# Kernel tuning notes

Hardware: AMD Instinct MI355X
Metric: run time of the kernel (lower is better)

The kernel has to match this reference:

```python
import jax, jax.numpy as jnp
import numpy as np

N = 200000  # nodes
C = 256     # per-node feature dim

def setup_inputs() -> dict:
    key = jax.random.key(0)
    k1, k2, k3, k4, k5, k6, k7 = jax.random.split(key, 7)
    out1 = jax.random.normal(k1, (N, C), dtype=jnp.float32)
    out2 = jax.random.normal(k2, (N, C), dtype=jnp.float32)
    neighbour = jax.random.randint(k3, (N, 3), 0, N, dtype=jnp.int64)
    # Combination2: Conv1d(512,512,1) == Linear(512->512)
    W_comb = jax.random.normal(k4, (512, 2 * C), dtype=jnp.float32) * (1.0 / np.sqrt(2 * C))
    b_comb = jax.random.normal(k5, (512,), dtype=jnp.float32) * 0.01
    # Aggregation2: Conv1d(256,512,1) == Linear(256->512)
    W_agg = jax.random.normal(k6, (512, C), dtype=jnp.float32) * (1.0 / np.sqrt(C))
    b_agg = jax.random.normal(k7, (512,), dtype=jnp.float32) * 0.01
    return {"out1": out1, "out2": out2, "neighbour": neighbour,
            "W_comb": W_comb, "b_comb": b_comb, "W_agg": W_agg, "b_agg": b_agg}


def reference(out1, out2, neighbour, W_comb, b_comb, W_agg, b_agg):
    # Combination2: concat features then 1x1 conv (per-node linear)
    a1 = jnp.concatenate([out1, out2], axis=1)              # [N, 512]
    out3 = jnp.einsum('nc,oc->no', a1, W_comb) + b_comb     # [N, 512]

    # Aggregation2: mean of self + 3 gathered neighbors, then linear 256->512
    neigh_feats = jnp.take(out2, neighbour, axis=0)          # [N, 3, C]
    agg = (out2 + neigh_feats.sum(axis=1)) * 0.25            # [N, C]
    out4 = jnp.einsum('nc,oc->no', agg, W_agg) + b_agg       # [N, 512]
    return (out3, out4)
```

## Files before the change

### kernel.cpp

```cpp
#include <hip/hip_runtime.h>


typedef __bf16 bf16x8 __attribute__((ext_vector_type(8)));
typedef float f32x4 __attribute__((ext_vector_type(4)));

#define N_NODES 200000
#define BM 64
#define NTILES (N_NODES / BM)
#define ROWC 520
#define ROWA 264
#define GRID_B 2048

__device__ __forceinline__ unsigned short f2bf(float x) {
  union { float f; unsigned int u; } v; v.f = x;
  return (unsigned short)((v.u + 0x7FFFu + ((v.u >> 16) & 1u)) >> 16);
}

__device__ __forceinline__ void st_bf4(unsigned short* p, float4 f) {
  uint2 w;
  w.x = (unsigned int)f2bf(f.x) | ((unsigned int)f2bf(f.y) << 16);
  w.y = (unsigned int)f2bf(f.z) | ((unsigned int)f2bf(f.w) << 16);
  *reinterpret_cast<uint2*>(p) = w;
}

__global__ void pack_w_kernel(const float* __restrict__ Wc,
                              const float* __restrict__ Wa,
                              unsigned short* __restrict__ Pc,
                              unsigned short* __restrict__ Pa) {
  int t = blockIdx.x * 256 + threadIdx.x;
  if (t >= (512 + 256) * 64) return;
  int lane = t & 63;
  int tile = t >> 6;
  const float* W;
  unsigned short* P;
  int K, kt_n;
  if (tile < 512) { W = Wc; P = Pc; K = 512; kt_n = 16; }
  else { tile -= 512; W = Wa; P = Pa; K = 256; kt_n = 8; }
  int nt = tile / kt_n;
  int kt = tile - nt * kt_n;
  int row = nt * 16 + (lane & 15);
  int k0 = kt * 32 + (lane >> 4) * 8;
  const float* src = W + (size_t)row * K + k0;
  unsigned short* dst = P + (size_t)tile * 512 + lane * 8;
#pragma unroll
  for (int j = 0; j < 8; ++j) dst[j] = f2bf(src[j]);
}

__global__ __launch_bounds__(512, 4) void gemm_kernel(
    const float* __restrict__ out1, const float* __restrict__ out2,
    const unsigned short* __restrict__ Pc, const unsigned short* __restrict__ Pa,
    const float* __restrict__ b_comb,
    float* __restrict__ out3, unsigned short* __restrict__ Y) {
  __shared__ unsigned short Acomb[BM * ROWC];

  const int tid = threadIdx.x;
  const int ln8 = tid >> 3, c8 = tid & 7;
  const int wave = tid >> 6, lane = tid & 63;
  const int l15 = lane & 15, l4 = lane >> 4;
  const long long node0 = (long long)blockIdx.x * BM;

  float bcv[4];
#pragma unroll
  for (int n = 0; n < 4; ++n) bcv[n] = b_comb[wave * 64 + n * 16 + l15];

  {
    const size_t gn = (size_t)node0 + ln8;
    const float4* r1 = reinterpret_cast<const float4*>(out1 + gn * 256);
    const float4* r2 = reinterpret_cast<const float4*>(out2 + gn * 256);
#pragma unroll
    for (int r = 0; r < 8; ++r) {
      const int cc = c8 + 8 * r;
      st_bf4(&Acomb[ln8 * ROWC + cc * 4], r1[cc]);
      st_bf4(&Acomb[ln8 * ROWC + 256 + cc * 4], r2[cc]);
    }
  }
  __syncthreads();

  const int nt0 = wave * 4;

  {
    f32x4 acc[4][4];
#pragma unroll
    for (int m = 0; m < 4; ++m)
#pragma unroll
      for (int n = 0; n < 4; ++n) acc[m][n] = (f32x4){0.f, 0.f, 0.f, 0.f};

    const unsigned short* pc = Pc + (size_t)nt0 * 16 * 512 + lane * 8;
    const unsigned short* ab = &Acomb[(size_t)l15 * ROWC + l4 * 8];
#pragma unroll
    for (int kt = 0; kt < 16; ++kt) {
      bf16x8 bfr[4];
#pragma unroll
      for (int n = 0; n < 4; ++n)
        bfr[n] = *reinterpret_cast<const bf16x8*>(pc + ((size_t)n * 16 + kt) * 512);
      bf16x8 av[4];
#pragma unroll
      for (int m = 0; m < 4; ++m)
        av[m] = *reinterpret_cast<const bf16x8*>(ab + (size_t)m * 16 * ROWC + kt * 32);
#pragma unroll
      for (int m = 0; m < 4; ++m)
#pragma unroll
        for (int n = 0; n < 4; ++n)
          acc[m][n] = __builtin_amdgcn_mfma_f32_16x16x32_bf16(av[m], bfr[n], acc[m][n], 0, 0, 0);
    }
    float* o3 = out3 + node0 * 512 + wave * 64 + l15;
#pragma unroll
    for (int m = 0; m < 4; ++m)
#pragma unroll
      for (int r = 0; r < 4; ++r) {
        float* p = o3 + (long long)(m * 16 + l4 * 4 + r) * 512;
#pragma unroll
        for (int n = 0; n < 4; ++n) p[n * 16] = acc[m][n][r] + bcv[n];
      }
  }

  {
    f32x4 acc[4][4];
#pragma unroll
    for (int m = 0; m < 4; ++m)
#pragma unroll
      for (int n = 0; n < 4; ++n) acc[m][n] = (f32x4){0.f, 0.f, 0.f, 0.f};

    const unsigned short* pa = Pa + (size_t)nt0 * 8 * 512 + lane * 8;
    const unsigned short* ab = &Acomb[(size_t)l15 * ROWC + 256 + l4 * 8];
#pragma unroll
    for (int kt = 0; kt < 8; ++kt) {
      bf16x8 bfr[4];
#pragma unroll
      for (int n = 0; n < 4; ++n)
        bfr[n] = *reinterpret_cast<const bf16x8*>(pa + ((size_t)n * 8 + kt) * 512);
      bf16x8 av[4];
#pragma unroll
      for (int m = 0; m < 4; ++m)
        av[m] = *reinterpret_cast<const bf16x8*>(ab + (size_t)m * 16 * ROWC + kt * 32);
#pragma unroll
      for (int m = 0; m < 4; ++m)
#pragma unroll
        for (int n = 0; n < 4; ++n)
          acc[m][n] = __builtin_amdgcn_mfma_f32_16x16x32_bf16(av[m], bfr[n], acc[m][n], 0, 0, 0);
    }

    __syncthreads();
#pragma unroll
    for (int m = 0; m < 4; ++m)
#pragma unroll
      for (int r = 0; r < 4; ++r) {
        const int row = m * 16 + l4 * 4 + r;
#pragma unroll
        for (int n = 0; n < 4; ++n)
          Acomb[row * ROWC + wave * 64 + n * 16 + l15] = f2bf(acc[m][n][r]);
      }
    __syncthreads();

    {
      const unsigned short* src = &Acomb[ln8 * ROWC];
      unsigned short* dst = Y + (node0 + ln8) * 512;
#pragma unroll
      for (int j = 0; j < 8; ++j) {
        const int e = (c8 + 8 * j) * 8;
        *reinterpret_cast<uint4*>(dst + e) = *reinterpret_cast<const uint4*>(src + e);
      }
    }
  }
}

__device__ __forceinline__ float bf_lo(unsigned u) {
  union { unsigned x; float f; } c; c.x = u << 16; return c.f;
}
__device__ __forceinline__ float bf_hi(unsigned u) {
  union { unsigned x; float f; } c; c.x = u & 0xFFFF0000u; return c.f;
}

__global__ __launch_bounds__(256) void gather_kernel(
    const unsigned short* __restrict__ Y, const int* __restrict__ nbr,
    const float* __restrict__ b_agg, float* __restrict__ out4) {
  const int lane = threadIdx.x & 63;
  const int wid = (blockIdx.x * 256 + threadIdx.x) >> 6;
  const int nwaves = (GRID_B * 256) >> 6;

  float ba[8];
  const float* bp = b_agg + lane * 8;
#pragma unroll
  for (int j = 0; j < 8; ++j) ba[j] = bp[j];

  for (int n = wid; n < N_NODES; n += nwaves) {
    int i0 = nbr[3 * n + 0];
    int i1 = nbr[3 * n + 1];
    int i2 = nbr[3 * n + 2];
    i0 = i0 < 0 ? 0 : (i0 >= N_NODES ? N_NODES - 1 : i0);
    i1 = i1 < 0 ? 0 : (i1 >= N_NODES ? N_NODES - 1 : i1);
    i2 = i2 < 0 ? 0 : (i2 >= N_NODES ? N_NODES - 1 : i2);

    const uint4 a  = *reinterpret_cast<const uint4*>(Y + (size_t)n  * 512 + lane * 8);
    const uint4 b0 = *reinterpret_cast<const uint4*>(Y + (size_t)i0 * 512 + lane * 8);
    const uint4 b1 = *reinterpret_cast<const uint4*>(Y + (size_t)i1 * 512 + lane * 8);
    const uint4 b2 = *reinterpret_cast<const uint4*>(Y + (size_t)i2 * 512 + lane * 8);

    const unsigned wa[4] = {a.x, a.y, a.z, a.w};
    const unsigned w0[4] = {b0.x, b0.y, b0.z, b0.w};
    const unsigned w1[4] = {b1.x, b1.y, b1.z, b1.w};
    const unsigned w2[4] = {b2.x, b2.y, b2.z, b2.w};
    float s[8];
#pragma unroll
    for (int w = 0; w < 4; ++w) {
      s[2 * w]     = bf_lo(wa[w]) + bf_lo(w0[w]) + bf_lo(w1[w]) + bf_lo(w2[w]);
      s[2 * w + 1] = bf_hi(wa[w]) + bf_hi(w0[w]) + bf_hi(w1[w]) + bf_hi(w2[w]);
    }
    f32x4 o0 = {s[0] * 0.25f + ba[0], s[1] * 0.25f + ba[1],
                s[2] * 0.25f + ba[2], s[3] * 0.25f + ba[3]};
    f32x4 o1 = {s[4] * 0.25f + ba[4], s[5] * 0.25f + ba[5],
                s[6] * 0.25f + ba[6], s[7] * 0.25f + ba[7]};
    f32x4* op = reinterpret_cast<f32x4*>(out4 + (size_t)n * 512 + lane * 8);
    __builtin_nontemporal_store(o0, op);
    __builtin_nontemporal_store(o1, op + 1);
  }
}

__global__ __launch_bounds__(512, 4) void mesh_fused_fallback(
    const float* __restrict__ out1, const float* __restrict__ out2,
    const int* __restrict__ nbr,
    const unsigned short* __restrict__ Pc, const unsigned short* __restrict__ Pa,
    const float* __restrict__ b_comb, const float* __restrict__ b_agg,
    float* __restrict__ outp) {
  __shared__ unsigned short Ac[32 * ROWC];
  __shared__ unsigned short Aagg[32 * ROWA];
  const int tid = threadIdx.x;
  const long long node0 = (long long)blockIdx.x * 32;
  {
    const int ln = tid >> 4, c16 = tid & 15;
    const long long gn = node0 + ln;
    long long i0 = nbr[3 * gn + 0], i1 = nbr[3 * gn + 1], i2 = nbr[3 * gn + 2];
    i0 = i0 < 0 ? 0 : (i0 >= N_NODES ? N_NODES - 1 : i0);
    i1 = i1 < 0 ? 0 : (i1 >= N_NODES ? N_NODES - 1 : i1);
    i2 = i2 < 0 ? 0 : (i2 >= N_NODES ? N_NODES - 1 : i2);
    const float4* r1 = reinterpret_cast<const float4*>(out1 + gn * 256);
    const float4* r2 = reinterpret_cast<const float4*>(out2 + gn * 256);
    const float4* g0 = reinterpret_cast<const float4*>(out2 + i0 * 256);
    const float4* g1 = reinterpret_cast<const float4*>(out2 + i1 * 256);
    const float4* g2 = reinterpret_cast<const float4*>(out2 + i2 * 256);
#pragma unroll
    for (int r = 0; r < 4; ++r) {
      const int c = c16 + 16 * r;
      float4 f1 = r1[c], f2 = r2[c], n0 = g0[c], n1 = g1[c], n2 = g2[c];
      float4 ag;
      ag.x = (f2.x + n0.x + n1.x + n2.x) * 0.25f;
      ag.y = (f2.y + n0.y + n1.y + n2.y) * 0.25f;
      ag.z = (f2.z + n0.z + n1.z + n2.z) * 0.25f;
      ag.w = (f2.w + n0.w + n1.w + n2.w) * 0.25f;
      st_bf4(&Ac[ln * ROWC + c * 4], f1);
      st_bf4(&Ac[ln * ROWC + 256 + c * 4], f2);
      st_bf4(&Aagg[ln * ROWA + c * 4], ag);
    }
  }
  __syncthreads();
  const int wave = tid >> 6, lane = tid & 63;
  const int l15 = lane & 15, l4 = lane >> 4;
  const int nt0 = wave * 4;
  float* o3 = outp;
  float* o4 = outp + (size_t)N_NODES * 512;
  {
    f32x4 acc[2][4];
#pragma unroll
    for (int m = 0; m < 2; ++m)
#pragma unroll
      for (int n = 0; n < 4; ++n) acc[m][n] = (f32x4){0.f, 0.f, 0.f, 0.f};
    const unsigned short* pc = Pc + (size_t)nt0 * 16 * 512 + lane * 8;
    const unsigned short* ab = &Ac[(size_t)l15 * ROWC + l4 * 8];
#pragma unroll
    for (int kt = 0; kt < 16; ++kt) {
      bf16x8 a0 = *reinterpret_cast<const bf16x8*>(ab + kt * 32);
      bf16x8 a1 = *reinterpret_cast<const bf16x8*>(ab + 16 * ROWC + kt * 32);
#pragma unroll
      for (int n = 0; n < 4; ++n) {
        bf16x8 b = *reinterpret_cast<const bf16x8*>(pc + ((size_t)n * 16 + kt) * 512);
        acc[0][n] = __builtin_amdgcn_mfma_f32_16x16x32_bf16(a0, b, acc[0][n], 0, 0, 0);
        acc[1][n] = __builtin_amdgcn_mfma_f32_16x16x32_bf16(a1, b, acc[1][n], 0, 0, 0);
      }
    }
#pragma unroll
    for (int m = 0; m < 2; ++m)
#pragma unroll
      for (int r = 0; r < 4; ++r)
#pragma unroll
        for (int n = 0; n < 4; ++n) {
          const int col = wave * 64 + n * 16 + l15;
          o3[(node0 + m * 16 + l4 * 4 + r) * 512 + col] = acc[m][n][r] + b_comb[col];
        }
  }
  {
    f32x4 acc[2][4];
#pragma unroll
    for (int m = 0; m < 2; ++m)
#pragma unroll
      for (int n = 0; n < 4; ++n) acc[m][n] = (f32x4){0.f, 0.f, 0.f, 0.f};
    const unsigned short* pa = Pa + (size_t)nt0 * 8 * 512 + lane * 8;
    const unsigned short* ab = &Aagg[(size_t)l15 * ROWA + l4 * 8];
#pragma unroll
    for (int kt = 0; kt < 8; ++kt) {
      bf16x8 a0 = *reinterpret_cast<const bf16x8*>(ab + kt * 32);
      bf16x8 a1 = *reinterpret_cast<const bf16x8*>(ab + 16 * ROWA + kt * 32);
#pragma unroll
      for (int n = 0; n < 4; ++n) {
        bf16x8 b = *reinterpret_cast<const bf16x8*>(pa + ((size_t)n * 8 + kt) * 512);
        acc[0][n] = __builtin_amdgcn_mfma_f32_16x16x32_bf16(a0, b, acc[0][n], 0, 0, 0);
        acc[1][n] = __builtin_amdgcn_mfma_f32_16x16x32_bf16(a1, b, acc[1][n], 0, 0, 0);
      }
    }
#pragma unroll
    for (int m = 0; m < 2; ++m)
#pragma unroll
      for (int r = 0; r < 4; ++r)
#pragma unroll
        for (int n = 0; n < 4; ++n) {
          const int col = wave * 64 + n * 16 + l15;
          o4[(node0 + m * 16 + l4 * 4 + r) * 512 + col] = acc[m][n][r] + b_agg[col];
        }
  }
}

extern "C" void kernel_launch(void* const* d_in, const int* in_sizes, int n_in,
                              void* d_out, int out_size, void* d_ws, size_t ws_size,
                              hipStream_t stream) {
  const float* out1 = (const float*)d_in[0];
  const float* out2 = (const float*)d_in[1];
  const int* nbr = (const int*)d_in[2];
  const float* Wc = (const float*)d_in[3];
  const float* bc = (const float*)d_in[4];
  const float* Wa = (const float*)d_in[5];
  const float* ba = (const float*)d_in[6];

  const size_t yElems = (size_t)N_NODES * 512;
  const size_t packElems = 512 * 512 + 512 * 256;
  const size_t need = (yElems + packElems) * 2;

  if (ws_size >= need) {
    unsigned short* Yw = (unsigned short*)d_ws;
    unsigned short* Pc = Yw + yElems;
    unsigned short* Pa = Pc + 512 * 512;
    pack_w_kernel<<<192, 256, 0, stream>>>(Wc, Wa, Pc, Pa);
    gemm_kernel<<<NTILES, 512, 0, stream>>>(out1, out2, Pc, Pa, bc, (float*)d_out, Yw);
    gather_kernel<<<GRID_B, 256, 0, stream>>>(Yw, nbr, ba,
                                              (float*)d_out + (size_t)N_NODES * 512);
  } else {
    unsigned short* Pc = (unsigned short*)d_ws;
    unsigned short* Pa = Pc + 512 * 512;
    pack_w_kernel<<<192, 256, 0, stream>>>(Wc, Wa, Pc, Pa);
    mesh_fused_fallback<<<N_NODES / 32, 512, 0, stream>>>(out1, out2, nbr, Pc, Pa, bc, ba,
                                                          (float*)d_out);
  }
}
```

Before: 519.9 us.

## Pipeline A-tile staging in K-chunks with double-buffered LDS and smaller row tile

The GEMM kernel now processes 32-row tiles and stages the activations in four 128-column phases through a double-buffered LDS array. Global loads for the next phase are issued while the current phase runs its MFMAs, and the combination and aggregation GEMMs share the A fragments of the out2 phases. The aim is to overlap global loads with matrix math and shrink LDS use, at the cost of more blocks, more B-weight reloads per row, and a lower occupancy hint. The Y tile is written back in two 16-row chunks through LDS.

```diff
diff --git a/kernel.cpp b/kernel.cpp
--- a/kernel.cpp
+++ b/kernel.cpp
@@ -5,8 +5,9 @@
 typedef float f32x4 __attribute__((ext_vector_type(4)));
 
 #define N_NODES 200000
-#define BM 64
+#define BM 32
 #define NTILES (N_NODES / BM)
+#define LDW 136
 #define ROWC 520
 #define ROWA 264
 #define GRID_B 2048
@@ -46,120 +47,103 @@
   for (int j = 0; j < 8; ++j) dst[j] = f2bf(src[j]);
 }
 
-__global__ __launch_bounds__(512, 4) void gemm_kernel(
+__global__ __launch_bounds__(512, 2) void gemm_kernel(
     const float* __restrict__ out1, const float* __restrict__ out2,
     const unsigned short* __restrict__ Pc, const unsigned short* __restrict__ Pa,
     const float* __restrict__ b_comb,
     float* __restrict__ out3, unsigned short* __restrict__ Y) {
-  __shared__ unsigned short Acomb[BM * ROWC];
+  __shared__ unsigned short lds[2][BM][LDW];
 
   const int tid = threadIdx.x;
-  const int ln8 = tid >> 3, c8 = tid & 7;
+  const int srow = tid >> 4, sc = tid & 15;
   const int wave = tid >> 6, lane = tid & 63;
   const int l15 = lane & 15, l4 = lane >> 4;
   const long long node0 = (long long)blockIdx.x * BM;
+  const int nt0 = wave * 4;
 
   float bcv[4];
 #pragma unroll
   for (int n = 0; n < 4; ++n) bcv[n] = b_comb[wave * 64 + n * 16 + l15];
 
+  f32x4 acc3[2][4], accY[2][4];
+#pragma unroll
+  for (int m = 0; m < 2; ++m)
+#pragma unroll
+    for (int n = 0; n < 4; ++n) {
+      acc3[m][n] = (f32x4){0.f, 0.f, 0.f, 0.f};
+      accY[m][n] = (f32x4){0.f, 0.f, 0.f, 0.f};
+    }
+
+  float4 sA, sB;
+  auto ldphase = [&](int p) {
+    const float* s = (p < 2 ? out1 : out2) + (node0 + srow) * 256 + (p & 1) * 128 + sc * 8;
+    sA = *reinterpret_cast<const float4*>(s);
+    sB = *reinterpret_cast<const float4*>(s + 4);
+  };
+
+  ldphase(0);
+
+#pragma unroll
+  for (int p = 0; p < 4; ++p) {
+    st_bf4(&lds[p & 1][srow][sc * 8], sA);
+    st_bf4(&lds[p & 1][srow][sc * 8 + 4], sB);
+    if (p < 3) ldphase(p + 1);
+    asm volatile("s_waitcnt lgkmcnt(0)" ::: "memory");
+    __builtin_amdgcn_s_barrier();
+
+#pragma unroll
+    for (int kt = 0; kt < 4; ++kt) {
+      bf16x8 a0 = *reinterpret_cast<const bf16x8*>(&lds[p & 1][l15][kt * 32 + l4 * 8]);
+      bf16x8 a1 = *reinterpret_cast<const bf16x8*>(&lds[p & 1][l15 + 16][kt * 32 + l4 * 8]);
+#pragma unroll
+      for (int n = 0; n < 4; ++n) {
+        bf16x8 b =
+            *reinterpret_cast<const bf16x8*>(Pc + ((size_t)(nt0 + n) * 16 + p * 4 + kt) * 512 + lane * 8);
+        acc3[0][n] = __builtin_amdgcn_mfma_f32_16x16x32_bf16(a0, b, acc3[0][n], 0, 0, 0);
+        acc3[1][n] = __builtin_amdgcn_mfma_f32_16x16x32_bf16(a1, b, acc3[1][n], 0, 0, 0);
+      }
+      if (p >= 2) {
+#pragma unroll
+        for (int n = 0; n < 4; ++n) {
+          bf16x8 b =
+              *reinterpret_cast<const bf16x8*>(Pa + ((size_t)(nt0 + n) * 8 + (p - 2) * 4 + kt) * 512 + lane * 8);
+          accY[0][n] = __builtin_amdgcn_mfma_f32_16x16x32_bf16(a0, b, accY[0][n], 0, 0, 0);
+          accY[1][n] = __builtin_amdgcn_mfma_f32_16x16x32_bf16(a1, b, accY[1][n], 0, 0, 0);
+        }
+      }
+    }
+  }
+
   {
-    const size_t gn = (size_t)node0 + ln8;
-    const float4* r1 = reinterpret_cast<const float4*>(out1 + gn * 256);
-    const float4* r2 = reinterpret_cast<const float4*>(out2 + gn * 256);
-#pragma unroll
-    for (int r = 0; r < 8; ++r) {
-      const int cc = c8 + 8 * r;
-      st_bf4(&Acomb[ln8 * ROWC + cc * 4], r1[cc]);
-      st_bf4(&Acomb[ln8 * ROWC + 256 + cc * 4], r2[cc]);
-    }
-  }
-  __syncthreads();
-
-  const int nt0 = wave * 4;
-
-  {
-    f32x4 acc[4][4];
-#pragma unroll
-    for (int m = 0; m < 4; ++m)
-#pragma unroll
-      for (int n = 0; n < 4; ++n) acc[m][n] = (f32x4){0.f, 0.f, 0.f, 0.f};
-
-    const unsigned short* pc = Pc + (size_t)nt0 * 16 * 512 + lane * 8;
-    const unsigned short* ab = &Acomb[(size_t)l15 * ROWC + l4 * 8];
-#pragma unroll
-    for (int kt = 0; kt < 16; ++kt) {
-      bf16x8 bfr[4];
+    float* o3 = out3 + node0 * 512 + wave * 64 + l15;
+#pragma unroll
+    for (int m = 0; m < 2; ++m)
+#pragma unroll
+      for (int r = 0; r < 4; ++r) {
+        float* pp = o3 + (long long)(m * 16 + l4 * 4 + r) * 512;
+#pragma unroll
+        for (int n = 0; n < 4; ++n) pp[n * 16] = acc3[m][n][r] + bcv[n];
+      }
+  }
+
+  unsigned short* yl = &lds[0][0][0];
+#pragma unroll
+  for (int ch = 0; ch < 2; ++ch) {
+    __syncthreads();
+#pragma unroll
+    for (int r = 0; r < 4; ++r) {
+      const int rl = l4 * 4 + r;
 #pragma unroll
       for (int n = 0; n < 4; ++n)
-        bfr[n] = *reinterpret_cast<const bf16x8*>(pc + ((size_t)n * 16 + kt) * 512);
-      bf16x8 av[4];
-#pragma unroll
-      for (int m = 0; m < 4; ++m)
-        av[m] = *reinterpret_cast<const bf16x8*>(ab + (size_t)m * 16 * ROWC + kt * 32);
-#pragma unroll
-      for (int m = 0; m < 4; ++m)
-#pragma unroll
-        for (int n = 0; n < 4; ++n)
-          acc[m][n] = __builtin_amdgcn_mfma_f32_16x16x32_bf16(av[m], bfr[n], acc[m][n], 0, 0, 0);
-    }
-    float* o3 = out3 + node0 * 512 + wave * 64 + l15;
-#pragma unroll
-    for (int m = 0; m < 4; ++m)
-#pragma unroll
-      for (int r = 0; r < 4; ++r) {
-        float* p = o3 + (long long)(m * 16 + l4 * 4 + r) * 512;
-#pragma unroll
-        for (int n = 0; n < 4; ++n) p[n * 16] = acc[m][n][r] + bcv[n];
-      }
-  }
-
-  {
-    f32x4 acc[4][4];
-#pragma unroll
-    for (int m = 0; m < 4; ++m)
-#pragma unroll
-      for (int n = 0; n < 4; ++n) acc[m][n] = (f32x4){0.f, 0.f, 0.f, 0.f};
-
-    const unsigned short* pa = Pa + (size_t)nt0 * 8 * 512 + lane * 8;
-    const unsigned short* ab = &Acomb[(size_t)l15 * ROWC + 256 + l4 * 8];
-#pragma unroll
-    for (int kt = 0; kt < 8; ++kt) {
-      bf16x8 bfr[4];
-#pragma unroll
-      for (int n = 0; n < 4; ++n)
-        bfr[n] = *reinterpret_cast<const bf16x8*>(pa + ((size_t)n * 8 + kt) * 512);
-      bf16x8 av[4];
-#pragma unroll
-      for (int m = 0; m < 4; ++m)
-        av[m] = *reinterpret_cast<const bf16x8*>(ab + (size_t)m * 16 * ROWC + kt * 32);
-#pragma unroll
-      for (int m = 0; m < 4; ++m)
-#pragma unroll
-        for (int n = 0; n < 4; ++n)
-          acc[m][n] = __builtin_amdgcn_mfma_f32_16x16x32_bf16(av[m], bfr[n], acc[m][n], 0, 0, 0);
-    }
-
+        yl[rl * 520 + wave * 64 + n * 16 + l15] = f2bf(accY[ch][n][r]);
+    }
     __syncthreads();
 #pragma unroll
-    for (int m = 0; m < 4; ++m)
-#pragma unroll
-      for (int r = 0; r < 4; ++r) {
-        const int row = m * 16 + l4 * 4 + r;
-#pragma unroll
-        for (int n = 0; n < 4; ++n)
-          Acomb[row * ROWC + wave * 64 + n * 16 + l15] = f2bf(acc[m][n][r]);
-      }
-    __syncthreads();
-
-    {
-      const unsigned short* src = &Acomb[ln8 * ROWC];
-      unsigned short* dst = Y + (node0 + ln8) * 512;
-#pragma unroll
-      for (int j = 0; j < 8; ++j) {
-        const int e = (c8 + 8 * j) * 8;
-        *reinterpret_cast<uint4*>(dst + e) = *reinterpret_cast<const uint4*>(src + e);
-      }
+    for (int q = 0; q < 2; ++q) {
+      const int idx = q * 512 + tid;
+      const int row = idx >> 6, c = idx & 63;
+      *reinterpret_cast<uint4*>(Y + (node0 + ch * 16 + row) * 512 + c * 8) =
+          *reinterpret_cast<const uint4*>(yl + row * 520 + c * 8);
     }
   }
 }
```

After: 896.4 us. 72.4% more time.
